# Optimization experiments

Measured on AMD Instinct MI355X. Metric: run time of the kernel, lower is better.

## Reference

```python
import math
import jax, jax.numpy as jnp
import numpy as np

H, D_MODEL, D_K, D_V, SEQ, BATCH = 12, 768, 64, 64, 2048, 4


def setup_inputs() -> dict:
    key = jax.random.key(0)
    k1, k2, k3, k4, k5 = jax.random.split(key, 5)
    s = math.sqrt(0.02)
    return {
        "residual": jax.random.normal(k1, (BATCH, SEQ, D_MODEL), dtype=jnp.float32),
        "W_Q": jax.random.normal(k2, (H, D_MODEL, D_K), dtype=jnp.float32) * s,
        "W_K": jax.random.normal(k3, (H, D_MODEL, D_K), dtype=jnp.float32) * s,
        "W_V": jax.random.normal(k4, (H, D_MODEL, D_V), dtype=jnp.float32) * s,
        "W_O": jax.random.normal(k5, (H * D_V, D_MODEL), dtype=jnp.float32) * s,
    }


def reference(residual, W_Q, W_K, W_V, W_O):
    B, S, _ = residual.shape
    # Projections: h=head, m=d_model, k=d_k/d_v
    Q = jnp.einsum("hmk,bsm->hbsk", W_Q, residual)
    K = jnp.einsum("hmk,bsm->hbsk", W_K, residual)
    V = jnp.einsum("hmv,bsm->hbsv", W_V, residual)
    # Scores [h, b, s_q, s_k] + additive causal mask, scaled BEFORE softmax
    QK = jnp.einsum("hbqk,hbsk->hbqs", Q, K)
    causal = jnp.triu(jnp.ones((S, S), dtype=bool), k=1)
    mask = jnp.where(causal, -jnp.inf, 0.0).astype(QK.dtype)  # broadcasts over h,b
    soft = jax.nn.softmax((QK + mask) / math.sqrt(D_K), axis=-1)
    attn = jnp.einsum("hbqs,hbsv->hbqv", soft, V)
    # [h,b,q,v] -> [b,q,h*v]
    multi_head = jnp.transpose(attn, (1, 2, 0, 3)).reshape(B, S, -1)
    return jnp.einsum("nd,bqn->bqd", W_O, multi_head)
```

## Files before the change

kernel.cpp:

```cpp
#include <hip/hip_runtime.h>

typedef _Float16 f16;
typedef _Float16 f16x8 __attribute__((ext_vector_type(8)));
typedef float f32x4 __attribute__((ext_vector_type(4)));

#define H_ 12
#define B_ 4
#define S_ 2048
#define DM 768
#define DK 64
#define HBSD ((size_t)H_ * B_ * S_ * DK)

__device__ __forceinline__ f16 f2h(float f) { return (f16)f; }

__device__ __forceinline__ void gl_lds16(const f16* g, f16* l) {
  __builtin_amdgcn_global_load_lds(
      (const __attribute__((address_space(1))) void*)g,
      (__attribute__((address_space(3))) void*)l, 16, 0, 0);
}


__global__ __launch_bounds__(256) void cast_x_kernel(const float* __restrict__ x,
                                                     f16* __restrict__ xb, int n4) {
  int i = blockIdx.x * 256 + threadIdx.x;
  if (i < n4) {
    float4 v = ((const float4*)x)[i];
    union { f16 h[4]; uint2 u; } pk;
    pk.h[0] = f2h(v.x); pk.h[1] = f2h(v.y); pk.h[2] = f2h(v.z); pk.h[3] = f2h(v.w);
    ((uint2*)xb)[i] = pk.u;
  }
}

__global__ __launch_bounds__(256) void tcast_qkv_kernel(const float* __restrict__ WQ,
                                                        const float* __restrict__ WK,
                                                        const float* __restrict__ WV,
                                                        f16* __restrict__ Wt) {
  __shared__ float L[64][65];
  const int m0 = blockIdx.x * 64, which = blockIdx.y, h = blockIdx.z;
  const float* in = (which == 0 ? WQ : which == 1 ? WK : WV) + (size_t)h * DM * DK;
  const int t = threadIdx.x;
  const int lr = t >> 2, lc = (t & 3) * 16;
  const float* ip = in + (size_t)(m0 + lr) * DK + lc;
#pragma unroll
  for (int i = 0; i < 4; i++) {
    float4 v = *(const float4*)(ip + i * 4);
    L[lr][lc + i * 4 + 0] = v.x;
    L[lr][lc + i * 4 + 1] = v.y;
    L[lr][lc + i * 4 + 2] = v.z;
    L[lr][lc + i * 4 + 3] = v.w;
  }
  __syncthreads();
  const int oc = t >> 2, om = (t & 3) * 16;
  union { f16 hh[16]; uint4 u[2]; } pk;
#pragma unroll
  for (int jx = 0; jx < 16; jx++) pk.hh[jx] = f2h(L[om + jx][oc]);
  f16* op = Wt + ((size_t)which * DM + h * DK + oc) * DM + m0 + om;
  *(uint4*)op = pk.u[0];
  *(uint4*)(op + 8) = pk.u[1];
}

__global__ __launch_bounds__(256) void tcast_wo_kernel(const float* __restrict__ WO,
                                                       f16* __restrict__ Wt) {
  __shared__ float L[64][65];
  const int n0 = blockIdx.x * 64, d0 = blockIdx.y * 64;
  const int t = threadIdx.x;
  const int lr = t >> 2, lc = (t & 3) * 16;
  const float* ip = WO + (size_t)(n0 + lr) * DM + d0 + lc;
#pragma unroll
  for (int i = 0; i < 4; i++) {
    float4 v = *(const float4*)(ip + i * 4);
    L[lr][lc + i * 4 + 0] = v.x;
    L[lr][lc + i * 4 + 1] = v.y;
    L[lr][lc + i * 4 + 2] = v.z;
    L[lr][lc + i * 4 + 3] = v.w;
  }
  __syncthreads();
  const int oc = t >> 2, om = (t & 3) * 16;
  union { f16 hh[16]; uint4 u[2]; } pk;
#pragma unroll
  for (int jx = 0; jx < 16; jx++) pk.hh[jx] = f2h(L[om + jx][oc]);
  f16* op = Wt + (size_t)(d0 + oc) * DM + n0 + om;
  *(uint4*)op = pk.u[0];
  *(uint4*)(op + 8) = pk.u[1];
}

template <int MODE>
__global__ __launch_bounds__(256) void gemm_bt_kernel(const f16* __restrict__ A,
                                                      const f16* __restrict__ Bt,
                                                      float* __restrict__ Cf,
                                                      f16* __restrict__ Cq,
                                                      f16* __restrict__ Vt, int N) {
  constexpr int K = 768;
  __shared__ __align__(16) f16 As[2 * 128 * 32];
  __shared__ __align__(16) f16 Bs[2 * 128 * 32];
  const int t = threadIdx.x;
  const int m0 = blockIdx.y * 128, n0 = blockIdx.x * 128;
  const int lane = t & 63, wave = t >> 6;
  const int l15 = lane & 15, quad = lane >> 4;
  const int m_off = (wave & 1) * 64, n_off = (wave >> 1) * 64;
  const int r0 = t >> 2, ko = (t & 3) * 8;
  const f16* Ag0 = A + (size_t)(m0 + r0) * K + ko;
  const f16* Ag1 = A + (size_t)(m0 + r0 + 64) * K + ko;
  const f16* Bg0 = Bt + (size_t)(n0 + r0) * K + ko;
  const f16* Bg1 = Bt + (size_t)(n0 + r0 + 64) * K + ko;

  f32x4 acc[4][4];
  const f32x4 z4 = {0.f, 0.f, 0.f, 0.f};
  for (int i = 0; i < 4; i++)
    for (int j = 0; j < 4; j++) acc[i][j] = z4;

  for (int kt = 0; kt < K; kt += 64) {
    __syncthreads();
#pragma unroll
    for (int s = 0; s < 2; s++) {
      gl_lds16(Ag0 + kt + s * 32, &As[s * 4096 + t * 8]);
      gl_lds16(Ag1 + kt + s * 32, &As[s * 4096 + 2048 + t * 8]);
      gl_lds16(Bg0 + kt + s * 32, &Bs[s * 4096 + t * 8]);
      gl_lds16(Bg1 + kt + s * 32, &Bs[s * 4096 + 2048 + t * 8]);
    }
    __syncthreads();
#pragma unroll
    for (int s = 0; s < 2; s++) {
      f16x8 af[4], bfr[4];
#pragma unroll
      for (int i = 0; i < 4; i++)
        af[i] = *(const f16x8*)&As[s * 4096 + (m_off + i * 16 + l15) * 32 + quad * 8];
#pragma unroll
      for (int i = 0; i < 4; i++)
        bfr[i] = *(const f16x8*)&Bs[s * 4096 + (n_off + i * 16 + l15) * 32 + quad * 8];
#pragma unroll
      for (int mi = 0; mi < 4; mi++)
#pragma unroll
        for (int ni = 0; ni < 4; ni++)
          acc[mi][ni] = __builtin_amdgcn_mfma_f32_16x16x32_f16(af[mi], bfr[ni],
                                                               acc[mi][ni], 0, 0, 0);
    }
  }

  if (MODE == 0) {
#pragma unroll
    for (int mi = 0; mi < 4; mi++) {
      int row = m0 + m_off + mi * 16 + quad * 4;
#pragma unroll
      for (int ni = 0; ni < 4; ni++) {
        int col = n0 + n_off + ni * 16 + l15;
#pragma unroll
        for (int r = 0; r < 4; r++) Cf[(size_t)(row + r) * N + col] = acc[mi][ni][r];
      }
    }
  } else {
#pragma unroll
    for (int mi = 0; mi < 4; mi++) {
      int srow = m0 + m_off + mi * 16 + quad * 4;
      int bb = srow >> 11, ss = srow & 2047;
#pragma unroll
      for (int ni = 0; ni < 4; ni++) {
        int n = n0 + n_off + ni * 16 + l15;
        int which = n / DM;
        int rr = n - which * DM;
        int h = rr >> 6, kk = rr & 63;
        if (which < 2) {
#pragma unroll
          for (int r = 0; r < 4; r++) {
            size_t dst = (size_t)which * HBSD +
                         ((size_t)((h * B_ + bb) * S_) + ss + r) * DK + kk;
            Cq[dst] = f2h(acc[mi][ni][r]);
          }
        } else {
          union { f16 hh[4]; uint2 u; } pk;
#pragma unroll
          for (int r = 0; r < 4; r++) pk.hh[r] = f2h(acc[mi][ni][r]);
          *(uint2*)&Vt[((size_t)(h * B_ + bb) * DK + kk) * S_ + ss] = pk.u;
        }
      }
    }
  }
}

__global__ __launch_bounds__(256, 3) void flash_kernel(const f16* __restrict__ Qg,
                                                       const f16* __restrict__ Kg,
                                                       const f16* __restrict__ Vtg,
                                                       f16* __restrict__ MH) {
  __shared__ __align__(16) f16 Ksh[2 * 64 * 32];
  __shared__ __align__(16) f16 Vsh[2 * 64 * 32];
  __shared__ __align__(16) f16 Ps[4][16 * 72];

  const int t = threadIdx.x, lane = t & 63, w = t >> 6;
  const int l15 = lane & 15, quad = lane >> 4;
  const int bid = blockIdx.x;
  const int xcd = bid & 7, gi = bid >> 3;
  const int hbi = gi % 6, pr = gi / 6;
  const int hb = xcd * 6 + hbi;
  const int qbA = pr, qbB = 31 - pr;
  const int h = hb >> 2, b = hb & 3;
  const size_t base = (size_t)hb * S_ * DK;
  const f16* Qp = Qg + base;
  const f16* Kp = Kg + base;
  const f16* Vp = Vtg + base;
  const float c2 = 0.18033688011f;

  f16x8 aqA[2], aqB[2];
  {
    const f16* qa = Qp + (size_t)(qbA * 64 + w * 16 + l15) * DK + quad * 8;
    aqA[0] = *(const f16x8*)(qa);
    aqA[1] = *(const f16x8*)(qa + 32);
    const f16* qb_ = Qp + (size_t)(qbB * 64 + w * 16 + l15) * DK + quad * 8;
    aqB[0] = *(const f16x8*)(qb_);
    aqB[1] = *(const f16x8*)(qb_ + 32);
  }
  const int qlaneA = qbA * 64 + w * 16 + l15;
  const int qlaneB = qbB * 64 + w * 16 + l15;

  const int srow = t >> 2, scol = (t & 3) * 8;
  const f16* Kst = Kp + (size_t)srow * DK + scol;
  const f16* Vst = Vp + (size_t)srow * S_ + scol;

  float mA = -1e30f, lA = 0.f, mB = -1e30f, lB = 0.f;
  f32x4 oA[4], oB[4];
  const f32x4 z4 = {0.f, 0.f, 0.f, 0.f};
#pragma unroll
  for (int ni = 0; ni < 4; ni++) { oA[ni] = z4; oB[ni] = z4; }

  auto do_job = [&](const f16x8* aq, float& m_s, float& l_s, f32x4* oacc,
                    int qlane, int kv0, bool diag) {
    f32x4 sa[4];
#pragma unroll
    for (int mi = 0; mi < 4; mi++) {
      f16x8 k0 = *(const f16x8*)&Ksh[(mi * 16 + l15) * 32 + quad * 8];
      sa[mi] = __builtin_amdgcn_mfma_f32_16x16x32_f16(k0, aq[0], z4, 0, 0, 0);
    }
#pragma unroll
    for (int mi = 0; mi < 4; mi++) {
      f16x8 k1 = *(const f16x8*)&Ksh[2048 + (mi * 16 + l15) * 32 + quad * 8];
      sa[mi] = __builtin_amdgcn_mfma_f32_16x16x32_f16(k1, aq[1], sa[mi], 0, 0, 0);
    }

    if (diag) {
#pragma unroll
      for (int mi = 0; mi < 4; mi++)
#pragma unroll
        for (int r = 0; r < 4; r++)
          if (kv0 + mi * 16 + quad * 4 + r > qlane) sa[mi][r] = -1e30f;
    }

    float mx = fmaxf(fmaxf(fmaxf(sa[0][0], sa[0][1]), fmaxf(sa[0][2], sa[0][3])),
                     fmaxf(fmaxf(sa[1][0], sa[1][1]), fmaxf(sa[1][2], sa[1][3])));
    float mx2 = fmaxf(fmaxf(fmaxf(sa[2][0], sa[2][1]), fmaxf(sa[2][2], sa[2][3])),
                      fmaxf(fmaxf(sa[3][0], sa[3][1]), fmaxf(sa[3][2], sa[3][3])));
    mx = fmaxf(mx, mx2);
    mx = fmaxf(mx, __shfl_xor(mx, 16));
    mx = fmaxf(mx, __shfl_xor(mx, 32));
    float m2old = m_s;
    float m2 = fmaxf(m2old, mx * c2);
    m_s = m2;
    float alpha = __builtin_exp2f(m2old - m2);
    float rs = 0.f;
#pragma unroll
    for (int mi = 0; mi < 4; mi++)
#pragma unroll
      for (int r = 0; r < 4; r++) {
        float p = __builtin_exp2f(fmaf(sa[mi][r], c2, -m2));
        sa[mi][r] = p;
        rs += p;
      }
    rs += __shfl_xor(rs, 16);
    rs += __shfl_xor(rs, 32);
    l_s = l_s * alpha + rs;

#pragma unroll
    for (int ni = 0; ni < 4; ni++)
#pragma unroll
      for (int r = 0; r < 4; r++) oacc[ni][r] *= alpha;

#pragma unroll
    for (int mi = 0; mi < 4; mi++) {
      union { f16 hh[4]; uint2 u; } pk;
#pragma unroll
      for (int r = 0; r < 4; r++) pk.hh[r] = f2h(sa[mi][r]);
      *(uint2*)&Ps[w][l15 * 72 + mi * 16 + quad * 4] = pk.u;
    }

#pragma unroll
    for (int kc2 = 0; kc2 < 2; kc2++) {
      f16x8 ap = *(const f16x8*)&Ps[w][l15 * 72 + kc2 * 32 + quad * 8];
#pragma unroll
      for (int ni = 0; ni < 4; ni++) {
        f16x8 vf = *(const f16x8*)&Vsh[kc2 * 2048 + (ni * 16 + l15) * 32 + quad * 8];
        oacc[ni] = __builtin_amdgcn_mfma_f32_16x16x32_f16(vf, ap, oacc[ni], 0, 0, 0);
      }
    }
  };

  for (int kt = 0; kt <= qbB; kt++) {
    const int kv0 = kt * 64;
    __syncthreads();
    gl_lds16(Kst + (size_t)kv0 * DK, &Ksh[t * 8]);
    gl_lds16(Kst + (size_t)kv0 * DK + 32, &Ksh[2048 + t * 8]);
    gl_lds16(Vst + kv0, &Vsh[t * 8]);
    gl_lds16(Vst + kv0 + 32, &Vsh[2048 + t * 8]);
    __syncthreads();

    do_job(aqB, mB, lB, oB, qlaneB, kv0, kt == qbB);
    if (kt <= qbA) do_job(aqA, mA, lA, oA, qlaneA, kv0, kt == qbA);
  }

  {
    float linv = 1.0f / lB;
    f16* dst = MH + ((size_t)b * S_ + qlaneB) * DM + h * DK + quad * 4;
#pragma unroll
    for (int ni = 0; ni < 4; ni++) {
      union { f16 hh[4]; uint2 u; } pk;
#pragma unroll
      for (int r = 0; r < 4; r++) pk.hh[r] = f2h(oB[ni][r] * linv);
      *(uint2*)(dst + ni * 16) = pk.u;
    }
  }
  {
    float linv = 1.0f / lA;
    f16* dst = MH + ((size_t)b * S_ + qlaneA) * DM + h * DK + quad * 4;
#pragma unroll
    for (int ni = 0; ni < 4; ni++) {
      union { f16 hh[4]; uint2 u; } pk;
#pragma unroll
      for (int r = 0; r < 4; r++) pk.hh[r] = f2h(oA[ni][r] * linv);
      *(uint2*)(dst + ni * 16) = pk.u;
    }
  }
}


extern "C" void kernel_launch(void* const* d_in, const int* in_sizes, int n_in,
                              void* d_out, int out_size, void* d_ws, size_t ws_size,
                              hipStream_t stream) {
  const float* residual = (const float*)d_in[0];
  const float* WQ = (const float*)d_in[1];
  const float* WK = (const float*)d_in[2];
  const float* WV = (const float*)d_in[3];
  const float* WO = (const float*)d_in[4];
  float* out = (float*)d_out;

  char* ws = (char*)d_ws;
  size_t off = 0;
  auto alloc = [&](size_t bytes) {
    void* p = ws + off;
    off += (bytes + 255) & ~(size_t)255;
    return p;
  };
  f16* xb = (f16*)alloc((size_t)B_ * S_ * DM * 2);
  f16* wqkv = (f16*)alloc((size_t)3 * DM * DM * 2);
  f16* wot = (f16*)alloc((size_t)DM * DM * 2);
  f16* qk = (f16*)alloc(2 * HBSD * 2);
  f16* vt = (f16*)alloc(HBSD * 2);
  f16* mh = (f16*)alloc((size_t)B_ * S_ * DM * 2);

  cast_x_kernel<<<(B_ * S_ * DM / 4 + 255) / 256, 256, 0, stream>>>(residual, xb,
                                                                    B_ * S_ * DM / 4);
  tcast_qkv_kernel<<<dim3(DM / 64, 3, H_), 256, 0, stream>>>(WQ, WK, WV, wqkv);
  tcast_wo_kernel<<<dim3(DM / 64, DM / 64), 256, 0, stream>>>(WO, wot);

  gemm_bt_kernel<1><<<dim3(3 * DM / 128, B_ * S_ / 128), 256, 0, stream>>>(
      xb, wqkv, nullptr, qk, vt, 3 * DM);

  flash_kernel<<<768, 256, 0, stream>>>(qk, qk + HBSD, vt, mh);

  gemm_bt_kernel<0><<<dim3(DM / 128, B_ * S_ / 128), 256, 0, stream>>>(
      mh, wot, out, nullptr, nullptr, DM);
}
```

Before: 223.9 us.

## Swizzle LDS tiles, add lazy softmax rescale, and use packed f16 conversion

XOR-swizzles the 16-byte column chunk of the K/V and GEMM LDS tiles, both where global_load_lds writes them and where fragments are read, to reduce LDS bank conflicts. In flash attention, the running max and the output/sum rescale are updated only when some lane's new max exceeds the stored max by more than 8 (in log2 units). This skips the per-tile exp and accumulator multiply in most iterations. P is now packed to f16 with cvt_pkrtz, which truncates toward zero and can let unnormalized probabilities grow up to 2^8 before they are converted.

```diff
diff --git a/kernel.cpp b/kernel.cpp
--- a/kernel.cpp
+++ b/kernel.cpp
@@ -1,6 +1,7 @@
 #include <hip/hip_runtime.h>
 
 typedef _Float16 f16;
+typedef __fp16 h16x2 __attribute__((ext_vector_type(2)));
 typedef _Float16 f16x8 __attribute__((ext_vector_type(8)));
 typedef float f32x4 __attribute__((ext_vector_type(4)));
 
@@ -97,8 +98,9 @@
   const int m0 = blockIdx.y * 128, n0 = blockIdx.x * 128;
   const int lane = t & 63, wave = t >> 6;
   const int l15 = lane & 15, quad = lane >> 4;
+  const int qsw = quad ^ ((l15 >> 1) & 3);
   const int m_off = (wave & 1) * 64, n_off = (wave >> 1) * 64;
-  const int r0 = t >> 2, ko = (t & 3) * 8;
+  const int r0 = t >> 2, ko = ((t & 3) ^ ((t >> 3) & 3)) * 8;
   const f16* Ag0 = A + (size_t)(m0 + r0) * K + ko;
   const f16* Ag1 = A + (size_t)(m0 + r0 + 64) * K + ko;
   const f16* Bg0 = Bt + (size_t)(n0 + r0) * K + ko;
@@ -124,10 +126,10 @@
       f16x8 af[4], bfr[4];
 #pragma unroll
       for (int i = 0; i < 4; i++)
-        af[i] = *(const f16x8*)&As[s * 4096 + (m_off + i * 16 + l15) * 32 + quad * 8];
+        af[i] = *(const f16x8*)&As[s * 4096 + (m_off + i * 16 + l15) * 32 + qsw * 8];
 #pragma unroll
       for (int i = 0; i < 4; i++)
-        bfr[i] = *(const f16x8*)&Bs[s * 4096 + (n_off + i * 16 + l15) * 32 + quad * 8];
+        bfr[i] = *(const f16x8*)&Bs[s * 4096 + (n_off + i * 16 + l15) * 32 + qsw * 8];
 #pragma unroll
       for (int mi = 0; mi < 4; mi++)
 #pragma unroll
@@ -187,6 +189,7 @@
 
   const int t = threadIdx.x, lane = t & 63, w = t >> 6;
   const int l15 = lane & 15, quad = lane >> 4;
+  const int qsw = quad ^ ((l15 >> 1) & 3);
   const int bid = blockIdx.x;
   const int xcd = bid & 7, gi = bid >> 3;
   const int hbi = gi % 6, pr = gi / 6;
@@ -211,7 +214,7 @@
   const int qlaneA = qbA * 64 + w * 16 + l15;
   const int qlaneB = qbB * 64 + w * 16 + l15;
 
-  const int srow = t >> 2, scol = (t & 3) * 8;
+  const int srow = t >> 2, scol = ((t & 3) ^ ((t >> 3) & 3)) * 8;
   const f16* Kst = Kp + (size_t)srow * DK + scol;
   const f16* Vst = Vp + (size_t)srow * S_ + scol;
 
@@ -226,12 +229,12 @@
     f32x4 sa[4];
 #pragma unroll
     for (int mi = 0; mi < 4; mi++) {
-      f16x8 k0 = *(const f16x8*)&Ksh[(mi * 16 + l15) * 32 + quad * 8];
+      f16x8 k0 = *(const f16x8*)&Ksh[(mi * 16 + l15) * 32 + qsw * 8];
       sa[mi] = __builtin_amdgcn_mfma_f32_16x16x32_f16(k0, aq[0], z4, 0, 0, 0);
     }
 #pragma unroll
     for (int mi = 0; mi < 4; mi++) {
-      f16x8 k1 = *(const f16x8*)&Ksh[2048 + (mi * 16 + l15) * 32 + quad * 8];
+      f16x8 k1 = *(const f16x8*)&Ksh[2048 + (mi * 16 + l15) * 32 + qsw * 8];
       sa[mi] = __builtin_amdgcn_mfma_f32_16x16x32_f16(k1, aq[1], sa[mi], 0, 0, 0);
     }
 
@@ -250,10 +253,18 @@
     mx = fmaxf(mx, mx2);
     mx = fmaxf(mx, __shfl_xor(mx, 16));
     mx = fmaxf(mx, __shfl_xor(mx, 32));
-    float m2old = m_s;
-    float m2 = fmaxf(m2old, mx * c2);
-    m_s = m2;
-    float alpha = __builtin_exp2f(m2old - m2);
+    float pm = mx * c2;
+    if (!__all(pm <= m_s + 8.f)) {
+      float m2 = fmaxf(m_s, pm);
+      float alpha = __builtin_exp2f(m_s - m2);
+      l_s *= alpha;
+#pragma unroll
+      for (int ni = 0; ni < 4; ni++)
+#pragma unroll
+        for (int r = 0; r < 4; r++) oacc[ni][r] *= alpha;
+      m_s = m2;
+    }
+    const float m2 = m_s;
     float rs = 0.f;
 #pragma unroll
     for (int mi = 0; mi < 4; mi++)
@@ -265,18 +276,13 @@
       }
     rs += __shfl_xor(rs, 16);
     rs += __shfl_xor(rs, 32);
-    l_s = l_s * alpha + rs;
-
-#pragma unroll
-    for (int ni = 0; ni < 4; ni++)
-#pragma unroll
-      for (int r = 0; r < 4; r++) oacc[ni][r] *= alpha;
-
-#pragma unroll
-    for (int mi = 0; mi < 4; mi++) {
-      union { f16 hh[4]; uint2 u; } pk;
-#pragma unroll
-      for (int r = 0; r < 4; r++) pk.hh[r] = f2h(sa[mi][r]);
+    l_s += rs;
+
+#pragma unroll
+    for (int mi = 0; mi < 4; mi++) {
+      union { h16x2 h2[2]; uint2 u; } pk;
+      pk.h2[0] = __builtin_amdgcn_cvt_pkrtz(sa[mi][0], sa[mi][1]);
+      pk.h2[1] = __builtin_amdgcn_cvt_pkrtz(sa[mi][2], sa[mi][3]);
       *(uint2*)&Ps[w][l15 * 72 + mi * 16 + quad * 4] = pk.u;
     }
 
@@ -285,7 +291,7 @@
       f16x8 ap = *(const f16x8*)&Ps[w][l15 * 72 + kc2 * 32 + quad * 8];
 #pragma unroll
       for (int ni = 0; ni < 4; ni++) {
-        f16x8 vf = *(const f16x8*)&Vsh[kc2 * 2048 + (ni * 16 + l15) * 32 + quad * 8];
+        f16x8 vf = *(const f16x8*)&Vsh[kc2 * 2048 + (ni * 16 + l15) * 32 + qsw * 8];
         oacc[ni] = __builtin_amdgcn_mfma_f32_16x16x32_f16(vf, ap, oacc[ni], 0, 0, 0);
       }
     }
```

Result: faster. 217.3 us (-2.9%).
